# Kernel tuning notes

Hardware: AMD Instinct MI355X
Metric: run time of the kernel (lower is better)

Reference implementation:

```python
import jax, jax.numpy as jnp
import numpy as np

D, H, DK, L, FF = 512, 8, 64, 6, 2048
MAXREL = 512
R = 2 * MAXREL + 1
B, S = 4, 512


def _ln(x, g, b):
    m = jnp.mean(x, -1, keepdims=True)
    v = jnp.mean((x - m) ** 2, -1, keepdims=True)
    return (x - m) * jax.lax.rsqrt(v + 1e-5) * g + b


def _gelu(x):
    return jax.nn.gelu(x, approximate=False)


def setup_inputs() -> dict:
    key = jax.random.key(0)
    ks = iter(jax.random.split(key, 64))
    def rnd(shape, scale=0.02):
        return jax.random.normal(next(ks), shape, jnp.float32) * scale
    inp = {"x": jax.random.normal(next(ks), (B, S, D), jnp.float32)}
    # SeasonalDecomposition params (3 seasonal nets stacked on leading axis)
    inp.update(
        sd_t1_w=rnd((D, D)), sd_t1_b=jnp.zeros((D,), jnp.float32),
        sd_t2_w=rnd((D, D)), sd_t2_b=jnp.zeros((D,), jnp.float32),
        sd_s1_w=rnd((3, D, D // 2)), sd_s1_b=jnp.zeros((3, D // 2), jnp.float32),
        sd_s2_w=rnd((3, D // 2, D)), sd_s2_b=jnp.zeros((3, D), jnp.float32),
        sd_r1_w=rnd((D, D // 2)), sd_r1_b=jnp.zeros((D // 2,), jnp.float32),
        sd_r2_w=rnd((D // 2, D)), sd_r2_b=jnp.zeros((D,), jnp.float32),
        sd_comb=jnp.ones((5,), jnp.float32),
        # 6 TemporalFusionTransformer layers, params stacked on leading axis L
        wq=rnd((L, D, D)), wk=rnd((L, D, D)), wv=rnd((L, D, D)),
        wo_w=rnd((L, D, D)), wo_b=jnp.zeros((L, D), jnp.float32),
        rel_k=rnd((L, R, DK), 1.0), rel_v=rnd((L, R, DK), 1.0),
        ln_attn_g=jnp.ones((L, D), jnp.float32), ln_attn_b=jnp.zeros((L, D), jnp.float32),
        ff1_w=rnd((L, D, FF)), ff1_b=jnp.zeros((L, FF), jnp.float32),
        ff2_w=rnd((L, FF, D)), ff2_b=jnp.zeros((L, D), jnp.float32),
        n1_g=jnp.ones((L, D), jnp.float32), n1_b=jnp.zeros((L, D), jnp.float32),
        n2_g=jnp.ones((L, D), jnp.float32), n2_b=jnp.zeros((L, D), jnp.float32),
    )
    return inp


def _forward(x, sd_t1_w, sd_t1_b, sd_t2_w, sd_t2_b, sd_s1_w, sd_s1_b, sd_s2_w, sd_s2_b,
             sd_r1_w, sd_r1_b, sd_r2_w, sd_r2_b, sd_comb,
             wq, wk, wv, wo_w, wo_b, rel_k, rel_v, ln_attn_g, ln_attn_b,
             ff1_w, ff1_b, ff2_w, ff2_b, n1_g, n1_b, n2_g, n2_b):
    b, s, d = x.shape
    # relative position index matrix, rp[i, j] = clip(j - i) + MAXREL
    r = jnp.arange(s)
    rp = jnp.clip(r[None, :] - r[:, None], -MAXREL, MAXREL) + MAXREL  # [S, S]

    # ---- SeasonalDecomposition (eval mode: dropout = identity) ----
    trend = _gelu(x @ sd_t1_w + sd_t1_b) @ sd_t2_w + sd_t2_b
    h = _gelu(jnp.einsum('bsd,kdm->kbsm', x, sd_s1_w) + sd_s1_b[:, None, None, :])
    seas = jnp.einsum('kbsm,kmd->kbsd', h, sd_s2_w) + sd_s2_b[:, None, None, :]  # [3,B,S,D]
    resid = _gelu(x @ sd_r1_w + sd_r1_b) @ sd_r2_w + sd_r2_b
    w = jax.nn.softmax(sd_comb)
    x = w[0] * trend + w[4] * resid + jnp.einsum('k,kbsd->bsd', w[1:4], seas)

    scale = np.float32(1.0 / np.sqrt(DK))

    def layer(xc, p):
        q = (xc @ p['wq']).reshape(b, s, H, DK).transpose(0, 2, 1, 3)  # [B,H,S,DK]
        k = (xc @ p['wk']).reshape(b, s, H, DK).transpose(0, 2, 1, 3)
        v = (xc @ p['wv']).reshape(b, s, H, DK).transpose(0, 2, 1, 3)
        scores = jnp.einsum('bhid,bhjd->bhij', q, k) * scale
        rk = p['rel_k'][rp]  # [S,S,DK] gathered rel-pos key bias
        scores = scores + jnp.einsum('bhid,ijd->bhij', q, rk)
        a = jax.nn.softmax(scores, axis=-1)
        ctx = jnp.einsum('bhij,bhjd->bhid', a, v)
        rv = p['rel_v'][rp]  # [S,S,DK]
        ctx = ctx + jnp.einsum('bhij,ijd->bhid', a, rv)
        ctx = ctx.transpose(0, 2, 1, 3).reshape(b, s, d)
        out = ctx @ p['wo_w'] + p['wo_b']
        attn = _ln(out + xc, p['ln_attn_g'], p['ln_attn_b'])
        y = _ln(xc + attn, p['n1_g'], p['n1_b'])
        ff = _gelu(y @ p['ff1_w'] + p['ff1_b']) @ p['ff2_w'] + p['ff2_b']
        y = _ln(y + ff, p['n2_g'], p['n2_b'])
        return y, None

    layers = dict(wq=wq, wk=wk, wv=wv, wo_w=wo_w, wo_b=wo_b, rel_k=rel_k, rel_v=rel_v,
                  ln_attn_g=ln_attn_g, ln_attn_b=ln_attn_b,
                  ff1_w=ff1_w, ff1_b=ff1_b, ff2_w=ff2_w, ff2_b=ff2_b,
                  n1_g=n1_g, n1_b=n1_b, n2_g=n2_g, n2_b=n2_b)
    x, _ = jax.lax.scan(layer, x, layers)
    return x


def reference(x, sd_t1_w, sd_t1_b, sd_t2_w, sd_t2_b, sd_s1_w, sd_s1_b, sd_s2_w, sd_s2_b,
              sd_r1_w, sd_r1_b, sd_r2_w, sd_r2_b, sd_comb,
              wq, wk, wv, wo_w, wo_b, rel_k, rel_v, ln_attn_g, ln_attn_b,
              ff1_w, ff1_b, ff2_w, ff2_b, n1_g, n1_b, n2_g, n2_b):
    return _forward(x, sd_t1_w, sd_t1_b, sd_t2_w, sd_t2_b, sd_s1_w, sd_s1_b, sd_s2_w, sd_s2_b,
                    sd_r1_w, sd_r1_b, sd_r2_w, sd_r2_b, sd_comb,
                    wq, wk, wv, wo_w, wo_b, rel_k, rel_v, ln_attn_g, ln_attn_b,
                    ff1_w, ff1_b, ff2_w, ff2_b, n1_g, n1_b, n2_g, n2_b)
```

## Files before the change

kernel.cpp:

```cpp
#include <hip/hip_runtime.h>
#include <hip/hip_bf16.h>

typedef __attribute__((ext_vector_type(4))) float f32x4;
typedef __attribute__((ext_vector_type(8))) short bf16x8;
typedef __attribute__((ext_vector_type(4))) short bf16x4;

#define NL 6

static __device__ __forceinline__ unsigned short f2bf(float f) {
    __hip_bfloat16 h = __float2bfloat16(f);
    return *reinterpret_cast<unsigned short*>(&h);
}
static __device__ __forceinline__ float bf2f(unsigned short u) {
    union { unsigned int u32; float f; } c; c.u32 = ((unsigned int)u) << 16; return c.f;
}
static __device__ __forceinline__ float gelu_exact(float v) {
    return 0.5f * v * (1.0f + erff(v * 0.70710678118654752f));
}
static __device__ __forceinline__ void gload_lds16(const void* g, void* l) {
    __builtin_amdgcn_global_load_lds((const __attribute__((address_space(1))) void*)g,
                                     (__attribute__((address_space(3))) void*)l, 16, 0, 0);
}
static __device__ __forceinline__ f32x4 MF(bf16x8 a, bf16x8 b, f32x4 c) {
    return __builtin_amdgcn_mfma_f32_16x16x32_bf16(a, b, c, 0, 0, 0);
}

template<int BM, int BN, bool OBF, bool BIAS, bool GACT, bool SPART, bool DUAL, bool VTR>
__global__ __launch_bounds__(256)
void gemm3(const unsigned short* __restrict__ A, const unsigned short* __restrict__ B,
           void* __restrict__ C, unsigned short* __restrict__ C2,
           const float* __restrict__ bias,
           int M, int N, int nkt, int skN, int lda, int ldb, int ldc, float alpha,
           int modA, long sA1, long sA2, int modB, long sB1, long sB2,
           int modC, long sC1, long sC2, int biasStride, long pStride)
{
    constexpr int MI = BM / 32, NI = BN / 32;
    constexpr int ACH = BM / 8, NCH = (BM + BN) / 8;
    __shared__ __attribute__((aligned(16))) unsigned short Ls[(BM + BN) * 64];

    const int bz = blockIdx.z;
    const int sk = SPART ? (bz % skN) : 0;
    const int z  = SPART ? (bz / skN) : bz;
    const unsigned short* Ab = A + (long)(z % modA) * sA1 + (long)(z / modA) * sA2;
    const unsigned short* Bb = B + (long)(z % modB) * sB1 + (long)(z / modB) * sB2;
    const long offC = (long)(z % modC) * sC1 + (long)(z / modC) * sC2;

    const int bm0 = blockIdx.x * BM, bn0 = blockIdx.y * BN;
    const int t = threadIdx.x, lane = t & 63, w = t >> 6;
    const int wm = (w >> 1) * (BM / 2), wn = (w & 1) * (BN / 2);
    const int crow8 = lane >> 3, cs8 = lane & 7;
    const int fr = lane & 15, kq = lane >> 4;
    const int kBase = sk * nkt * 64;

    f32x4 acc[MI][NI];
    #pragma unroll
    for (int a = 0; a < MI; a++)
        #pragma unroll
        for (int b = 0; b < NI; b++) acc[a][b] = (f32x4){0.f, 0.f, 0.f, 0.f};

    for (int kt = 0; kt < nkt; ++kt) {
        const int k0 = kBase + (kt << 6);
        #pragma unroll
        for (int c0 = 0; c0 < NCH; c0 += 4) {
            int c = c0 + w;
            if (c < NCH) {
                const unsigned short* gp;
                if (c < ACH) {
                    int rit = c * 8 + crow8;
                    int ks = cs8 ^ (rit & 7);
                    gp = Ab + (long)(bm0 + rit) * lda + k0 + ks * 8;
                } else {
                    int rit = (c - ACH) * 8 + crow8;
                    int ks = cs8 ^ (rit & 7);
                    gp = Bb + (long)(bn0 + rit) * ldb + k0 + ks * 8;
                }
                gload_lds16(gp, &Ls[c * 512]);
            }
        }
        __syncthreads();
        bf16x8 af[2][MI], bfr[2][NI];
        #pragma unroll
        for (int mi = 0; mi < MI; mi++) {
            int R = wm + mi * 16 + fr;
            af[0][mi] = *(const bf16x8*)&Ls[R * 64 + ((kq ^ (R & 7)) << 3)];
            af[1][mi] = *(const bf16x8*)&Ls[R * 64 + (((4 + kq) ^ (R & 7)) << 3)];
        }
        #pragma unroll
        for (int ni = 0; ni < NI; ni++) {
            int Rb = wn + ni * 16 + fr;
            bfr[0][ni] = *(const bf16x8*)&Ls[BM * 64 + Rb * 64 + ((kq ^ (Rb & 7)) << 3)];
            bfr[1][ni] = *(const bf16x8*)&Ls[BM * 64 + Rb * 64 + (((4 + kq) ^ (Rb & 7)) << 3)];
        }
        #pragma unroll
        for (int kh = 0; kh < 2; kh++)
            #pragma unroll
            for (int mi = 0; mi < MI; mi++)
                #pragma unroll
                for (int ni = 0; ni < NI; ni++)
                    acc[mi][ni] = MF(af[kh][mi], bfr[kh][ni], acc[mi][ni]);
        __syncthreads();
    }

    const int q4 = (lane >> 4) << 2;
    if (VTR && bn0 >= 1024) {
        #pragma unroll
        for (int mi = 0; mi < MI; mi++)
            #pragma unroll
            for (int ni = 0; ni < NI; ni++)
                #pragma unroll
                for (int j = 0; j < 4; j++) {
                    int lr = wm + mi * 16 + q4 + j;
                    int lc = wn + ni * 16 + fr;
                    Ls[lc * 64 + ((((lr >> 4) ^ (lc & 3)) << 4) | (lr & 15))] = f2bf(acc[mi][ni][j]);
                }
        __syncthreads();
        int dl = t >> 2, c4 = (t & 3) << 4;
        const unsigned short* src = &Ls[dl * 64 + (((t & 3) ^ (dl & 3)) << 4)];
        unsigned short* dst = C2 + ((long)((bm0 >> 9) * 8 + ((bn0 - 1024) >> 6)) * 64 + dl) * 512
                              + (bm0 & 511) + c4;
        *(bf16x8*)dst = *(const bf16x8*)src;
        *((bf16x8*)dst + 1) = *((const bf16x8*)src + 1);
    } else if (SPART) {
        float* P = (float*)C + sk * pStride + offC;
        #pragma unroll
        for (int mi = 0; mi < MI; mi++)
            #pragma unroll
            for (int ni = 0; ni < NI; ni++)
                #pragma unroll
                for (int j = 0; j < 4; j++) {
                    int gr = bm0 + wm + mi * 16 + q4 + j;
                    int gc = bn0 + wn + ni * 16 + fr;
                    if (gc < N) P[(long)gr * ldc + gc] = acc[mi][ni][j] * alpha;
                }
    } else {
        float* Cf = (float*)C + offC;
        unsigned short* Ch = (unsigned short*)C + offC;
        unsigned short* C2h = DUAL ? (C2 + offC) : nullptr;
        const float* bp = BIAS ? (bias + (long)z * biasStride) : nullptr;
        #pragma unroll
        for (int mi = 0; mi < MI; mi++)
            #pragma unroll
            for (int ni = 0; ni < NI; ni++)
                #pragma unroll
                for (int j = 0; j < 4; j++) {
                    int gr = bm0 + wm + mi * 16 + q4 + j;
                    int gc = bn0 + wn + ni * 16 + fr;
                    if (gc < N) {
                        float v = acc[mi][ni][j] * alpha;
                        if (BIAS) v += bp[gc];
                        if (GACT) v = gelu_exact(v);
                        if (OBF) Ch[(long)gr * ldc + gc] = f2bf(v);
                        else     Cf[(long)gr * ldc + gc] = v;
                        if (DUAL) C2h[(long)gr * ldc + gc] = f2bf(v);
                    }
                }
    }
}

__global__ __launch_bounds__(256)
void fused_attn3(const unsigned short* __restrict__ qkv,
                 const unsigned short* __restrict__ vt,
                 const unsigned short* __restrict__ rk,
                 const unsigned short* __restrict__ rvt,
                 unsigned short* __restrict__ ctx)
{
    __shared__ __attribute__((aligned(16))) unsigned short L[32768];
    const int bh = blockIdx.y, b = bh >> 3, h = bh & 7;
    const int i0 = blockIdx.x * 64;
    const int t = threadIdx.x, lane = t & 63, wv = t >> 6;
    const int crow = lane >> 2, cs = lane & 3;
    const int fr = lane & 15, kq = lane >> 4;
    const int q4 = kq << 2;
    const int iiw = wv * 16;
    const int PB = 20480, GA = 24576;

    const unsigned short* Qg = qkv + ((long)(b * 512 + i0)) * 1536 + h * 64;
    const unsigned short* Kg = qkv + ((long)(b * 512)) * 1536 + 512 + h * 64;
    const unsigned short* Vg = vt + ((long)bh * 64) * 512;

    auto stage = [&](int jt, int sbuf) {
        const int j0 = jt * 64;
        const int SB = 4096 + sbuf * 8192;
        #pragma unroll
        for (int k = 0; k < 4; k++) {
            int c = wv + k * 4;
            const unsigned short* gp; int dst;
            if (c < 8) {
                int kt = c >> 2, row = (c & 3) * 16 + crow, ks = cs ^ (row & 3);
                gp = Kg + (long)(j0 + row) * 1536 + kt * 32 + ks * 8;
                dst = SB + c * 512;
            } else {
                int cc = c - 8;
                int kt = cc >> 2, row = (cc & 3) * 16 + crow, ks = cs ^ (row & 3);
                gp = Vg + (long)row * 512 + j0 + kt * 32 + ks * 8;
                dst = SB + 4096 + cc * 512;
            }
            gload_lds16(gp, &L[dst]);
        }
    };

    #pragma unroll
    for (int k = 0; k < 2; k++) {
        int c = wv + k * 4;
        int kt = c >> 2, row = (c & 3) * 16 + crow, ks = cs ^ (row & 3);
        gload_lds16(Qg + (long)row * 1536 + kt * 32 + ks * 8, &L[c * 512]);
    }
    stage(0, 0);
    __syncthreads();
    bf16x8 qf[2];
    {
        int r = iiw + fr;
        qf[0] = *(const bf16x8*)&L[r * 32 + ((kq ^ (r & 3)) << 3)];
        qf[1] = *(const bf16x8*)&L[2048 + r * 32 + ((kq ^ (r & 3)) << 3)];
    }

    f32x4 ctxa[4];
    #pragma unroll
    for (int ni = 0; ni < 4; ni++) ctxa[ni] = (f32x4){0.f, 0.f, 0.f, 0.f};
    float m_[4] = {-1e30f, -1e30f, -1e30f, -1e30f};
    float l_[4] = {0.f, 0.f, 0.f, 0.f};

    for (int jt = 0; jt < 8; ++jt) {
        const int sb = jt & 1;
        const int SB = 4096 + sb * 8192;
        const int rbase = jt * 64 - i0 + 448;
        if (jt < 7) stage(jt + 1, sb ^ 1);
        f32x4 gacc[8];
        #pragma unroll
        for (int wb = 0; wb < 8; wb++) {
            int Rb = wb * 16 + fr;
            const unsigned short* rkp = rk + (long)(rbase + Rb) * 64 + kq * 8;
            bf16x8 rk0 = *(const bf16x8*)rkp;
            bf16x8 rk1 = *(const bf16x8*)(rkp + 32);
            f32x4 g = (f32x4){0.f, 0.f, 0.f, 0.f};
            g = MF(qf[0], rk0, g);
            gacc[wb] = MF(qf[1], rk1, g);
        }
        #pragma unroll
        for (int wb = 0; wb < 8; wb++)
            #pragma unroll
            for (int j = 0; j < 4; j++) {
                int il = iiw + q4 + j, ww = wb * 16 + fr;
                L[GA + il * 128 + (((ww >> 3) ^ (il & 7)) << 3) + (ww & 7)] = f2bf(gacc[wb][j]);
            }
        f32x4 s[4];
        #pragma unroll
        for (int ni = 0; ni < 4; ni++) {
            int rB = ni * 16 + fr;
            bf16x8 b0 = *(const bf16x8*)&L[SB + rB * 32 + ((kq ^ (rB & 3)) << 3)];
            bf16x8 b1 = *(const bf16x8*)&L[SB + 2048 + rB * 32 + ((kq ^ (rB & 3)) << 3)];
            f32x4 a0 = (f32x4){0.f, 0.f, 0.f, 0.f};
            a0 = MF(qf[0], b0, a0);
            s[ni] = MF(qf[1], b1, a0);
        }
        #pragma unroll
        for (int ni = 0; ni < 4; ni++)
            #pragma unroll
            for (int j = 0; j < 4; j++) {
                int il = iiw + q4 + j;
                int ww = ni * 16 + fr - il + 64;
                s[ni][j] = s[ni][j] * 0.125f
                         + bf2f(L[GA + il * 128 + (((ww >> 3) ^ (il & 7)) << 3) + (ww & 7)]);
            }
        float mx[4];
        #pragma unroll
        for (int j = 0; j < 4; j++) {
            mx[j] = fmaxf(fmaxf(s[0][j], s[1][j]), fmaxf(s[2][j], s[3][j]));
            #pragma unroll
            for (int msk = 1; msk < 16; msk <<= 1) mx[j] = fmaxf(mx[j], __shfl_xor(mx[j], msk));
        }
        float scl[4];
        #pragma unroll
        for (int j = 0; j < 4; j++) {
            float mn = fmaxf(m_[j], mx[j]);
            scl[j] = __expf(m_[j] - mn);
            m_[j] = mn;
        }
        float rs[4] = {0.f, 0.f, 0.f, 0.f};
        #pragma unroll
        for (int ni = 0; ni < 4; ni++)
            #pragma unroll
            for (int j = 0; j < 4; j++) {
                float p = __expf(s[ni][j] - m_[j]);
                s[ni][j] = p;
                rs[j] += p;
            }
        #pragma unroll
        for (int j = 0; j < 4; j++) {
            #pragma unroll
            for (int msk = 1; msk < 16; msk <<= 1) rs[j] += __shfl_xor(rs[j], msk);
            l_[j] = l_[j] * scl[j] + rs[j];
        }
        #pragma unroll
        for (int ni = 0; ni < 4; ni++)
            #pragma unroll
            for (int j = 0; j < 4; j++) ctxa[ni][j] *= scl[j];
        #pragma unroll
        for (int ni = 0; ni < 4; ni++)
            #pragma unroll
            for (int j = 0; j < 4; j++) {
                int il = iiw + q4 + j;
                int jj = ni * 16 + fr;
                unsigned short pb = f2bf(s[ni][j]);
                L[PB + il * 64 + (((jj >> 3) ^ (il & 7)) << 3) + (jj & 7)] = pb;
                int wI = jj - il + 64;
                L[GA + il * 128 + (((wI >> 3) ^ (il & 7)) << 3) + (wI & 7)] = pb;
                int wz = (wI + 64) & 127;
                L[GA + il * 128 + (((wz >> 3) ^ (il & 7)) << 3) + (wz & 7)] = 0;
            }
        bf16x8 rvf[4][4];
        #pragma unroll
        for (int kt2 = 0; kt2 < 4; kt2++)
            #pragma unroll
            for (int ni = 0; ni < 4; ni++)
                rvf[kt2][ni] = *(const bf16x8*)(rvt + (long)(ni * 16 + fr) * 1056
                                                + rbase + kt2 * 32 + kq * 8);
        const int r = iiw + fr;
        bf16x8 pa0 = *(const bf16x8*)&L[PB + r * 64 + ((kq ^ (r & 7)) << 3)];
        bf16x8 pa1 = *(const bf16x8*)&L[PB + r * 64 + (((4 + kq) ^ (r & 7)) << 3)];
        #pragma unroll
        for (int ni = 0; ni < 4; ni++) {
            int rB = ni * 16 + fr;
            bf16x8 vb0 = *(const bf16x8*)&L[SB + 4096 + rB * 32 + ((kq ^ (rB & 3)) << 3)];
            bf16x8 vb1 = *(const bf16x8*)&L[SB + 6144 + rB * 32 + ((kq ^ (rB & 3)) << 3)];
            ctxa[ni] = MF(pa0, vb0, ctxa[ni]);
            ctxa[ni] = MF(pa1, vb1, ctxa[ni]);
        }
        #pragma unroll
        for (int kt2 = 0; kt2 < 4; kt2++) {
            bf16x8 aa = *(const bf16x8*)&L[GA + r * 128 + (((kt2 * 4 + kq) ^ (r & 7)) << 3)];
            #pragma unroll
            for (int ni = 0; ni < 4; ni++)
                ctxa[ni] = MF(aa, rvf[kt2][ni], ctxa[ni]);
        }
        __syncthreads();
    }
    #pragma unroll
    for (int j = 0; j < 4; j++) {
        float inv = 1.f / l_[j];
        int il = iiw + q4 + j;
        unsigned short* op = ctx + ((long)(b * 512 + i0 + il)) * 512 + h * 64;
        #pragma unroll
        for (int ni = 0; ni < 4; ni++)
            op[ni * 16 + fr] = f2bf(ctxa[ni][j] * inv);
    }
}

__global__ __launch_bounds__(256)
void trcast_k(const float* __restrict__ in, unsigned short* __restrict__ out,
              int R, int C, int ldo, long inStride, long outStride,
              const float* __restrict__ scp, int sczs)
{
    __shared__ unsigned short tile[32][33];
    const int z = blockIdx.z;
    const float* ip = in + (long)z * inStride;
    unsigned short* op = out + (long)z * outStride;
    const float sc = scp ? scp[z * sczs] : 1.0f;
    const int c0 = blockIdx.x * 32, r0 = blockIdx.y * 32;
    const int tx = threadIdx.x & 31, ty = threadIdx.x >> 5;
    #pragma unroll
    for (int q = 0; q < 4; q++) {
        int r = r0 + ty + q * 8;
        float v = (r < R) ? ip[(long)r * C + c0 + tx] * sc : 0.f;
        tile[ty + q * 8][tx] = f2bf(v);
    }
    __syncthreads();
    #pragma unroll
    for (int q = 0; q < 4; q++) {
        int c = c0 + ty + q * 8;
        op[(long)c * ldo + r0 + tx] = tile[tx][ty + q * 8];
    }
}

__global__ __launch_bounds__(256)
void qkvwo_tr(const float* __restrict__ wq, const float* __restrict__ wk,
              const float* __restrict__ wv, const float* __restrict__ wo,
              unsigned short* __restrict__ qkvT, unsigned short* __restrict__ woT)
{
    __shared__ unsigned short tile[32][33];
    const int z = blockIdx.z;
    const int wsel = z / 6, l = z % 6;
    const float* ip = (wsel == 0 ? wq : wsel == 1 ? wk : wsel == 2 ? wv : wo) + (long)l * 262144;
    unsigned short* op = (wsel < 3) ? (qkvT + (long)l * 786432 + (long)wsel * 262144)
                                    : (woT + (long)l * 262144);
    const int c0 = blockIdx.x * 32, r0 = blockIdx.y * 32;
    const int tx = threadIdx.x & 31, ty = threadIdx.x >> 5;
    #pragma unroll
    for (int q = 0; q < 4; q++)
        tile[ty + q * 8][tx] = f2bf(ip[(long)(r0 + ty + q * 8) * 512 + c0 + tx]);
    __syncthreads();
    #pragma unroll
    for (int q = 0; q < 4; q++)
        op[(long)(c0 + ty + q * 8) * 512 + r0 + tx] = tile[tx][ty + q * 8];
}

__global__ __launch_bounds__(256)
void castpad_k(const float* __restrict__ in, unsigned short* __restrict__ out,
               int R, int C, long inStride, long outStride, long nPerZ)
{
    const int z = blockIdx.z;
    for (long idx = (long)blockIdx.x * 256 + threadIdx.x; idx < nPerZ;
         idx += (long)gridDim.x * 256) {
        int r = (int)(idx / C);
        float v = (r < R) ? in[(long)z * inStride + idx] : 0.f;
        out[(long)z * outStride + idx] = f2bf(v);
    }
}

__global__ __launch_bounds__(256)
void ln2x_k(const float* __restrict__ p0, const float* __restrict__ p1,
            const float* __restrict__ wb, const float* __restrict__ x,
            const float* __restrict__ g1, const float* __restrict__ b1,
            const float* __restrict__ g2, const float* __restrict__ b2,
            float* __restrict__ yf, unsigned short* __restrict__ yb)
{
    const int wv = threadIdx.x >> 6, lane = threadIdx.x & 63;
    const long row = (long)blockIdx.x * 4 + wv;
    const int base = lane * 8;
    const float* pa = p0 + row * 512 + base;
    const float* pbp = p1 + row * 512 + base;
    const float* px = x + row * 512 + base;
    float xv[8], v[8];
    {
        float4 x0 = *(const float4*)px, x1 = *(const float4*)(px + 4);
        float4 a0 = *(const float4*)pa, a1 = *(const float4*)(pa + 4);
        float4 c0 = *(const float4*)pbp, c1 = *(const float4*)(pbp + 4);
        float4 w0 = *(const float4*)(wb + base), w1 = *(const float4*)(wb + base + 4);
        xv[0] = x0.x; xv[1] = x0.y; xv[2] = x0.z; xv[3] = x0.w;
        xv[4] = x1.x; xv[5] = x1.y; xv[6] = x1.z; xv[7] = x1.w;
        v[0] = xv[0] + a0.x + c0.x + w0.x; v[1] = xv[1] + a0.y + c0.y + w0.y;
        v[2] = xv[2] + a0.z + c0.z + w0.z; v[3] = xv[3] + a0.w + c0.w + w0.w;
        v[4] = xv[4] + a1.x + c1.x + w1.x; v[5] = xv[5] + a1.y + c1.y + w1.y;
        v[6] = xv[6] + a1.z + c1.z + w1.z; v[7] = xv[7] + a1.w + c1.w + w1.w;
    }
    float s = 0.f;
    #pragma unroll
    for (int jj = 0; jj < 8; jj++) s += v[jj];
    #pragma unroll
    for (int off = 32; off; off >>= 1) s += __shfl_xor(s, off);
    float mean = s * (1.f / 512.f);
    float vs = 0.f;
    #pragma unroll
    for (int jj = 0; jj < 8; jj++) { float d = v[jj] - mean; vs += d * d; }
    #pragma unroll
    for (int off = 32; off; off >>= 1) vs += __shfl_xor(vs, off);
    float inv = rsqrtf(vs * (1.f / 512.f) + 1e-5f);
    float4 ga = *(const float4*)(g1 + base), gb = *(const float4*)(g1 + base + 4);
    float4 ba = *(const float4*)(b1 + base), bb = *(const float4*)(b1 + base + 4);
    float gg[8] = {ga.x, ga.y, ga.z, ga.w, gb.x, gb.y, gb.z, gb.w};
    float ee[8] = {ba.x, ba.y, ba.z, ba.w, bb.x, bb.y, bb.z, bb.w};
    float tvec[8];
    #pragma unroll
    for (int jj = 0; jj < 8; jj++) tvec[jj] = xv[jj] + (v[jj] - mean) * inv * gg[jj] + ee[jj];
    float s2 = 0.f;
    #pragma unroll
    for (int jj = 0; jj < 8; jj++) s2 += tvec[jj];
    #pragma unroll
    for (int off = 32; off; off >>= 1) s2 += __shfl_xor(s2, off);
    float m2 = s2 * (1.f / 512.f);
    float vs2 = 0.f;
    #pragma unroll
    for (int jj = 0; jj < 8; jj++) { float d = tvec[jj] - m2; vs2 += d * d; }
    #pragma unroll
    for (int off = 32; off; off >>= 1) vs2 += __shfl_xor(vs2, off);
    float inv2 = rsqrtf(vs2 * (1.f / 512.f) + 1e-5f);
    float4 gc = *(const float4*)(g2 + base), gd = *(const float4*)(g2 + base + 4);
    float4 bc = *(const float4*)(b2 + base), bd = *(const float4*)(b2 + base + 4);
    float g2v[8] = {gc.x, gc.y, gc.z, gc.w, gd.x, gd.y, gd.z, gd.w};
    float b2v[8] = {bc.x, bc.y, bc.z, bc.w, bd.x, bd.y, bd.z, bd.w};
    float r[8];
    #pragma unroll
    for (int jj = 0; jj < 8; jj++) r[jj] = (tvec[jj] - m2) * inv2 * g2v[jj] + b2v[jj];
    float* pf = yf + row * 512 + base;
    *(float4*)pf = (float4){r[0], r[1], r[2], r[3]};
    *(float4*)(pf + 4) = (float4){r[4], r[5], r[6], r[7]};
    bf16x8 ov;
    #pragma unroll
    for (int jj = 0; jj < 8; jj++) ov[jj] = (short)f2bf(r[jj]);
    *(bf16x8*)(yb + row * 512 + base) = ov;
}

__global__ __launch_bounds__(256)
void lnff_k(const float* __restrict__ y1, const float* __restrict__ parts,
            const float* __restrict__ bias,
            const float* __restrict__ g, const float* __restrict__ be,
            float* __restrict__ o, unsigned short* __restrict__ ob)
{
    const int wv = threadIdx.x >> 6, lane = threadIdx.x & 63;
    const long row = (long)blockIdx.x * 4 + wv;
    const int base = lane * 8;
    const float* pa = y1 + row * 512 + base;
    float v[8];
    {
        float4 x0 = *(const float4*)pa, x1 = *(const float4*)(pa + 4);
        float4 w0 = *(const float4*)(bias + base), w1 = *(const float4*)(bias + base + 4);
        v[0] = x0.x + w0.x; v[1] = x0.y + w0.y; v[2] = x0.z + w0.z; v[3] = x0.w + w0.w;
        v[4] = x1.x + w1.x; v[5] = x1.y + w1.y; v[6] = x1.z + w1.z; v[7] = x1.w + w1.w;
    }
    #pragma unroll
    for (int k = 0; k < 4; k++) {
        const float* pp = parts + (long)k * 1048576 + row * 512 + base;
        float4 a0 = *(const float4*)pp, a1 = *(const float4*)(pp + 4);
        v[0] += a0.x; v[1] += a0.y; v[2] += a0.z; v[3] += a0.w;
        v[4] += a1.x; v[5] += a1.y; v[6] += a1.z; v[7] += a1.w;
    }
    float s = 0.f;
    #pragma unroll
    for (int jj = 0; jj < 8; jj++) s += v[jj];
    #pragma unroll
    for (int off = 32; off; off >>= 1) s += __shfl_xor(s, off);
    float mean = s * (1.f / 512.f);
    float vs = 0.f;
    #pragma unroll
    for (int jj = 0; jj < 8; jj++) { float d = v[jj] - mean; vs += d * d; }
    #pragma unroll
    for (int off = 32; off; off >>= 1) vs += __shfl_xor(vs, off);
    float inv = rsqrtf(vs * (1.f / 512.f) + 1e-5f);
    float4 g0 = *(const float4*)(g + base), g1 = *(const float4*)(g + base + 4);
    float4 e0 = *(const float4*)(be + base), e1 = *(const float4*)(be + base + 4);
    float gg[8] = {g0.x, g0.y, g0.z, g0.w, g1.x, g1.y, g1.z, g1.w};
    float ee[8] = {e0.x, e0.y, e0.z, e0.w, e1.x, e1.y, e1.z, e1.w};
    float r[8];
    #pragma unroll
    for (int jj = 0; jj < 8; jj++) r[jj] = (v[jj] - mean) * inv * gg[jj] + ee[jj];
    float* po = o + row * 512 + base;
    *(float4*)po = (float4){r[0], r[1], r[2], r[3]};
    *(float4*)(po + 4) = (float4){r[4], r[5], r[6], r[7]};
    bf16x8 ov;
    #pragma unroll
    for (int jj = 0; jj < 8; jj++) ov[jj] = (short)f2bf(r[jj]);
    *(bf16x8*)(ob + row * 512 + base) = ov;
}

__global__ void softmax5_k(const float* __restrict__ comb, float* __restrict__ c5)
{
    if (threadIdx.x == 0 && blockIdx.x == 0) {
        float c[5]; float m = -1e30f;
        for (int k = 0; k < 5; k++) { c[k] = comb[k]; m = fmaxf(m, c[k]); }
        float s = 0.f;
        for (int k = 0; k < 5; k++) { c[k] = __expf(c[k] - m); s += c[k]; }
        for (int k = 0; k < 5; k++) c5[k] = c[k] / s;
    }
}

__global__ __launch_bounds__(256)
void bias_build_k(const float* __restrict__ t1b, const float* __restrict__ r1b,
                  const float* __restrict__ s1b, const float* __restrict__ t2b,
                  const float* __restrict__ r2b, const float* __restrict__ s2b,
                  const float* __restrict__ c5, float* __restrict__ b1c,
                  float* __restrict__ bc)
{
    int i = threadIdx.x + blockIdx.x * 256;
    if (i < 512) b1c[i] = t1b[i];
    else if (i < 768) b1c[i] = r1b[i - 512];
    else if (i < 1536) b1c[i] = s1b[i - 768];
    else if (i < 2048) {
        int n = i - 1536;
        bc[n] = c5[0] * t2b[n] + c5[4] * r2b[n]
              + c5[1] * s2b[n] + c5[2] * s2b[512 + n] + c5[3] * s2b[1024 + n];
    }
}

#define G3(BM,BN,OBF,BIAS,GACT,SPART,DUAL,VTR, A,B,C,C2,bias_, M,N,NKT,SKN, lda,ldb,ldc, alpha, mA,a1,a2, mB,b1,b2, mC,c1,c2, bstr, pstr, Zg) \
    gemm3<BM,BN,OBF,BIAS,GACT,SPART,DUAL,VTR><<<dim3((M)/(BM), ((N)+(BN)-1)/(BN), (Zg)), dim3(256), 0, stream>>>( \
        (A),(B),(C),(C2),(bias_),(M),(N),(NKT),(SKN),(lda),(ldb),(ldc),(alpha), \
        (mA),(long)(a1),(long)(a2),(mB),(long)(b1),(long)(b2),(mC),(long)(c1),(long)(c2),(bstr),(long)(pstr))

extern "C" void kernel_launch(void* const* d_in, const int* in_sizes, int n_in,
                              void* d_out, int out_size, void* d_ws, size_t ws_size,
                              hipStream_t stream)
{
    (void)in_sizes; (void)n_in; (void)out_size; (void)ws_size;
    const float* x    = (const float*)d_in[0];
    const float* t1w  = (const float*)d_in[1];
    const float* t1b  = (const float*)d_in[2];
    const float* t2w  = (const float*)d_in[3];
    const float* t2b  = (const float*)d_in[4];
    const float* s1w  = (const float*)d_in[5];
    const float* s1b  = (const float*)d_in[6];
    const float* s2w  = (const float*)d_in[7];
    const float* s2b  = (const float*)d_in[8];
    const float* r1w  = (const float*)d_in[9];
    const float* r1b  = (const float*)d_in[10];
    const float* r2w  = (const float*)d_in[11];
    const float* r2b  = (const float*)d_in[12];
    const float* comb = (const float*)d_in[13];
    const float* wq   = (const float*)d_in[14];
    const float* wk   = (const float*)d_in[15];
    const float* wvv  = (const float*)d_in[16];
    const float* wow  = (const float*)d_in[17];
    const float* wob  = (const float*)d_in[18];
    const float* relk = (const float*)d_in[19];
    const float* relv = (const float*)d_in[20];
    const float* lag  = (const float*)d_in[21];
    const float* labi = (const float*)d_in[22];
    const float* f1w  = (const float*)d_in[23];
    const float* f1b  = (const float*)d_in[24];
    const float* f2w  = (const float*)d_in[25];
    const float* f2b  = (const float*)d_in[26];
    const float* n1g  = (const float*)d_in[27];
    const float* n1b  = (const float*)d_in[28];
    const float* n2g  = (const float*)d_in[29];
    const float* n2b  = (const float*)d_in[30];

    char* ws = (char*)d_ws;
    #define OFFK(kb) (ws + (size_t)(kb) * 1024)
    float* X    = (float*)OFFK(0);
    float* T3   = (float*)OFFK(8192);
    float* PART = (float*)OFFK(12288);
    unsigned short* Xb   = (unsigned short*)OFFK(45056);
    unsigned short* Xb0  = (unsigned short*)OFFK(47104);
    unsigned short* QKVb = (unsigned short*)OFFK(49152);
    unsigned short* VT   = (unsigned short*)OFFK(55296);
    unsigned short* CTXb = (unsigned short*)OFFK(57344);
    unsigned short* T3b  = (unsigned short*)OFFK(59392);
    unsigned short* FFb  = (unsigned short*)OFFK(61440);
    unsigned short* W1   = (unsigned short*)OFFK(69632);
    unsigned short* W2   = (unsigned short*)OFFK(71168);
    float* b1c = (float*)OFFK(72704);
    float* bc  = (float*)OFFK(72712);
    float* c5  = (float*)OFFK(72716);
    unsigned short* qkvT = (unsigned short*)OFFK(119808);
    unsigned short* woT  = (unsigned short*)OFFK(129024);
    unsigned short* f1wT = (unsigned short*)OFFK(132096);
    unsigned short* f2wT = (unsigned short*)OFFK(144384);
    unsigned short* relkb= (unsigned short*)OFFK(156672);
    unsigned short* rvT  = (unsigned short*)OFFK(157488);
    unsigned short* Hb   = QKVb;

    castpad_k<<<dim3(1024, 1, 1), 256, 0, stream>>>(x, Xb0, 2048, 512, 1048576, 1048576, 1048576);
    softmax5_k<<<dim3(1), 64, 0, stream>>>(comb, c5);
    bias_build_k<<<dim3(8), 256, 0, stream>>>(t1b, r1b, s1b, t2b, r2b, s2b, c5, b1c, bc);
    trcast_k<<<dim3(16, 16, 1), 256, 0, stream>>>(t1w, W1, 512, 512, 512, 0, 0, nullptr, 0);
    trcast_k<<<dim3(8, 16, 1), 256, 0, stream>>>(r1w, W1 + 262144, 512, 256, 512, 0, 0, nullptr, 0);
    trcast_k<<<dim3(8, 16, 3), 256, 0, stream>>>(s1w, W1 + 393216, 512, 256, 512, 131072, 131072, nullptr, 0);
    trcast_k<<<dim3(16, 16, 1), 256, 0, stream>>>(t2w, W2, 512, 512, 1536, 0, 0, c5, 0);
    trcast_k<<<dim3(16, 8, 1), 256, 0, stream>>>(r2w, W2 + 512, 256, 512, 1536, 0, 0, c5 + 4, 0);
    trcast_k<<<dim3(16, 8, 3), 256, 0, stream>>>(s2w, W2 + 768, 256, 512, 1536, 131072, 256, c5 + 1, 1);
    qkvwo_tr<<<dim3(16, 16, 24), 256, 0, stream>>>(wq, wk, wvv, wow, qkvT, woT);
    trcast_k<<<dim3(64, 16, 6), 256, 0, stream>>>(f1w, f1wT, 512, 2048, 512, 1048576, 1048576, nullptr, 0);
    trcast_k<<<dim3(16, 64, 6), 256, 0, stream>>>(f2w, f2wT, 2048, 512, 2048, 1048576, 1048576, nullptr, 0);
    trcast_k<<<dim3(2, 33, 6), 256, 0, stream>>>(relv, rvT, 1025, 64, 1056, 65600, 67584, nullptr, 0);
    castpad_k<<<dim3(272, 1, 6), 256, 0, stream>>>(relk, relkb, 1025, 64, 65600, 69632, 69632);

    G3(64,64,true,true,true,false,false,false,  Xb0, W1, Hb, nullptr, b1c, 2048,1536,8,1, 512,512,1536, 1.f,
       1,0,0, 1,0,0, 1,0,0, 0,0, 1);
    G3(64,64,false,true,false,false,true,false, Hb, W2, X, Xb, bc, 2048,512,24,1, 1536,1536,512, 1.f,
       1,0,0, 1,0,0, 1,0,0, 0,0, 1);

    for (int l = 0; l < NL; ++l) {
        const unsigned short* qkvTl = qkvT + (long)l * 786432;
        const unsigned short* woTl  = woT + (long)l * 262144;
        const unsigned short* f1Tl  = f1wT + (long)l * 1048576;
        const unsigned short* f2Tl  = f2wT + (long)l * 1048576;
        const unsigned short* rkl   = relkb + (long)l * 69632;
        const unsigned short* rvl   = rvT + (long)l * 67584;

        G3(64,64,true,false,false,false,false,true, Xb, qkvTl, QKVb, VT, nullptr, 2048,1536,8,1, 512,512,1536, 1.f,
           1,0,0, 1,0,0, 1,0,0, 0,0, 1);
        fused_attn3<<<dim3(8, 32), 256, 0, stream>>>(QKVb, VT, rkl, rvl, CTXb);
        G3(64,64,false,false,false,true,false,false, CTXb, woTl, PART, nullptr, nullptr, 2048,512,4,2, 512,512,512, 1.f,
           1,0,0, 1,0,0, 1,0,0, 0,1048576, 2);
        ln2x_k<<<dim3(512), 256, 0, stream>>>(PART, PART + 1048576, wob + l * 512, X,
                                              lag + l * 512, labi + l * 512,
                                              n1g + l * 512, n1b + l * 512, T3, T3b);
        G3(64,64,true,true,true,false,false,false, T3b, f1Tl, FFb, nullptr, f1b + l * 2048, 2048,2048,8,1, 512,512,2048, 1.f,
           1,0,0, 1,0,0, 1,0,0, 0,0, 1);
        G3(64,64,false,false,false,true,false,false, FFb, f2Tl, PART, nullptr, nullptr, 2048,512,8,4, 2048,2048,512, 1.f,
           1,0,0, 1,0,0, 1,0,0, 0,1048576, 4);
        float* outp = (l == NL - 1) ? (float*)d_out : X;
        lnff_k<<<dim3(512), 256, 0, stream>>>(T3, PART, f2b + l * 512,
                                              n2g + l * 512, n2b + l * 512, outp, Xb);
    }
}
```

Before: 596.1 us.

## Split attention over key halves with merge kernel and stage relative tables in LDS

The attention kernel is split along the key dimension into two halves via a third grid dimension, doubling block count from 256 to 512. Each half writes unnormalized fp32 partial outputs plus running max and sum, and a new merge kernel combines them into the bf16 context. Relative-key and relative-value tables are now staged into LDS with async loads instead of being read directly from global memory. Double buffering is dropped in favour of single-buffer staging with two barriers per tile. The cost is an extra launch, fp32 partial traffic and loss of load/compute overlap.

```diff
diff --git a/kernel.cpp b/kernel.cpp
--- a/kernel.cpp
+++ b/kernel.cpp
@@ -158,42 +158,52 @@
 }
 
 __global__ __launch_bounds__(256)
-void fused_attn3(const unsigned short* __restrict__ qkv,
+void fused_attn4(const unsigned short* __restrict__ qkv,
                  const unsigned short* __restrict__ vt,
                  const unsigned short* __restrict__ rk,
                  const unsigned short* __restrict__ rvt,
-                 unsigned short* __restrict__ ctx)
-{
-    __shared__ __attribute__((aligned(16))) unsigned short L[32768];
+                 float* __restrict__ op, float* __restrict__ ml)
+{
+    __shared__ __attribute__((aligned(16))) unsigned short L[40960];
     const int bh = blockIdx.y, b = bh >> 3, h = bh & 7;
     const int i0 = blockIdx.x * 64;
+    const int half = blockIdx.z;
     const int t = threadIdx.x, lane = t & 63, wv = t >> 6;
     const int crow = lane >> 2, cs = lane & 3;
     const int fr = lane & 15, kq = lane >> 4;
     const int q4 = kq << 2;
     const int iiw = wv * 16;
-    const int PB = 20480, GA = 24576;
+    const int PB = 28672, GA = 32768;
 
     const unsigned short* Qg = qkv + ((long)(b * 512 + i0)) * 1536 + h * 64;
     const unsigned short* Kg = qkv + ((long)(b * 512)) * 1536 + 512 + h * 64;
     const unsigned short* Vg = vt + ((long)bh * 64) * 512;
 
-    auto stage = [&](int jt, int sbuf) {
-        const int j0 = jt * 64;
-        const int SB = 4096 + sbuf * 8192;
-        #pragma unroll
-        for (int k = 0; k < 4; k++) {
+    auto stage = [&](int jt) {
+        const int j0 = jt * 64, rbase = j0 - i0 + 448;
+        #pragma unroll
+        for (int k = 0; k < 12; k++) {
             int c = wv + k * 4;
             const unsigned short* gp; int dst;
             if (c < 8) {
                 int kt = c >> 2, row = (c & 3) * 16 + crow, ks = cs ^ (row & 3);
                 gp = Kg + (long)(j0 + row) * 1536 + kt * 32 + ks * 8;
-                dst = SB + c * 512;
-            } else {
+                dst = 4096 + c * 512;
+            } else if (c < 16) {
                 int cc = c - 8;
                 int kt = cc >> 2, row = (cc & 3) * 16 + crow, ks = cs ^ (row & 3);
                 gp = Vg + (long)row * 512 + j0 + kt * 32 + ks * 8;
-                dst = SB + 4096 + cc * 512;
+                dst = 8192 + cc * 512;
+            } else if (c < 32) {
+                int cc = c - 16;
+                int kt = cc >> 2, row = (cc & 3) * 16 + crow, ks = cs ^ (row & 3);
+                gp = rvt + (long)row * 1056 + rbase + kt * 32 + ks * 8;
+                dst = 12288 + cc * 512;
+            } else {
+                int cc = c - 32;
+                int kt = cc >> 3, row = (cc & 7) * 16 + crow, ks = cs ^ (row & 3);
+                gp = rk + (long)(rbase + row) * 64 + kt * 32 + ks * 8;
+                dst = 20480 + cc * 512;
             }
             gload_lds16(gp, &L[dst]);
         }
@@ -205,7 +215,7 @@
         int kt = c >> 2, row = (c & 3) * 16 + crow, ks = cs ^ (row & 3);
         gload_lds16(Qg + (long)row * 1536 + kt * 32 + ks * 8, &L[c * 512]);
     }
-    stage(0, 0);
+    stage(half * 4);
     __syncthreads();
     bf16x8 qf[2];
     {
@@ -220,18 +230,16 @@
     float m_[4] = {-1e30f, -1e30f, -1e30f, -1e30f};
     float l_[4] = {0.f, 0.f, 0.f, 0.f};
 
-    for (int jt = 0; jt < 8; ++jt) {
-        const int sb = jt & 1;
-        const int SB = 4096 + sb * 8192;
+    for (int q = 0; q < 4; ++q) {
+        const int jt = half * 4 + q;
         const int rbase = jt * 64 - i0 + 448;
-        if (jt < 7) stage(jt + 1, sb ^ 1);
+        (void)rbase;
         f32x4 gacc[8];
         #pragma unroll
         for (int wb = 0; wb < 8; wb++) {
             int Rb = wb * 16 + fr;
-            const unsigned short* rkp = rk + (long)(rbase + Rb) * 64 + kq * 8;
-            bf16x8 rk0 = *(const bf16x8*)rkp;
-            bf16x8 rk1 = *(const bf16x8*)(rkp + 32);
+            bf16x8 rk0 = *(const bf16x8*)&L[20480 + Rb * 32 + ((kq ^ (Rb & 3)) << 3)];
+            bf16x8 rk1 = *(const bf16x8*)&L[24576 + Rb * 32 + ((kq ^ (Rb & 3)) << 3)];
             f32x4 g = (f32x4){0.f, 0.f, 0.f, 0.f};
             g = MF(qf[0], rk0, g);
             gacc[wb] = MF(qf[1], rk1, g);
@@ -247,8 +255,8 @@
         #pragma unroll
         for (int ni = 0; ni < 4; ni++) {
             int rB = ni * 16 + fr;
-            bf16x8 b0 = *(const bf16x8*)&L[SB + rB * 32 + ((kq ^ (rB & 3)) << 3)];
-            bf16x8 b1 = *(const bf16x8*)&L[SB + 2048 + rB * 32 + ((kq ^ (rB & 3)) << 3)];
+            bf16x8 b0 = *(const bf16x8*)&L[4096 + rB * 32 + ((kq ^ (rB & 3)) << 3)];
+            bf16x8 b1 = *(const bf16x8*)&L[6144 + rB * 32 + ((kq ^ (rB & 3)) << 3)];
             f32x4 a0 = (f32x4){0.f, 0.f, 0.f, 0.f};
             a0 = MF(qf[0], b0, a0);
             s[ni] = MF(qf[1], b1, a0);
@@ -308,21 +316,14 @@
                 int wz = (wI + 64) & 127;
                 L[GA + il * 128 + (((wz >> 3) ^ (il & 7)) << 3) + (wz & 7)] = 0;
             }
-        bf16x8 rvf[4][4];
-        #pragma unroll
-        for (int kt2 = 0; kt2 < 4; kt2++)
-            #pragma unroll
-            for (int ni = 0; ni < 4; ni++)
-                rvf[kt2][ni] = *(const bf16x8*)(rvt + (long)(ni * 16 + fr) * 1056
-                                                + rbase + kt2 * 32 + kq * 8);
         const int r = iiw + fr;
         bf16x8 pa0 = *(const bf16x8*)&L[PB + r * 64 + ((kq ^ (r & 7)) << 3)];
         bf16x8 pa1 = *(const bf16x8*)&L[PB + r * 64 + (((4 + kq) ^ (r & 7)) << 3)];
         #pragma unroll
         for (int ni = 0; ni < 4; ni++) {
             int rB = ni * 16 + fr;
-            bf16x8 vb0 = *(const bf16x8*)&L[SB + 4096 + rB * 32 + ((kq ^ (rB & 3)) << 3)];
-            bf16x8 vb1 = *(const bf16x8*)&L[SB + 6144 + rB * 32 + ((kq ^ (rB & 3)) << 3)];
+            bf16x8 vb0 = *(const bf16x8*)&L[8192 + rB * 32 + ((kq ^ (rB & 3)) << 3)];
+            bf16x8 vb1 = *(const bf16x8*)&L[10240 + rB * 32 + ((kq ^ (rB & 3)) << 3)];
             ctxa[ni] = MF(pa0, vb0, ctxa[ni]);
             ctxa[ni] = MF(pa1, vb1, ctxa[ni]);
         }
@@ -330,20 +331,50 @@
         for (int kt2 = 0; kt2 < 4; kt2++) {
             bf16x8 aa = *(const bf16x8*)&L[GA + r * 128 + (((kt2 * 4 + kq) ^ (r & 7)) << 3)];
             #pragma unroll
-            for (int ni = 0; ni < 4; ni++)
-                ctxa[ni] = MF(aa, rvf[kt2][ni], ctxa[ni]);
-        }
-        __syncthreads();
-    }
+            for (int ni = 0; ni < 4; ni++) {
+                int rB = ni * 16 + fr;
+                bf16x8 rb = *(const bf16x8*)&L[12288 + kt2 * 2048 + rB * 32 + ((kq ^ (rB & 3)) << 3)];
+                ctxa[ni] = MF(aa, rb, ctxa[ni]);
+            }
+        }
+        if (q < 3) {
+            __syncthreads();
+            stage(jt + 1);
+            __syncthreads();
+        }
+    }
+    const long prow_base = (long)half * 16384 + (long)bh * 512 + i0;
     #pragma unroll
     for (int j = 0; j < 4; j++) {
-        float inv = 1.f / l_[j];
         int il = iiw + q4 + j;
-        unsigned short* op = ctx + ((long)(b * 512 + i0 + il)) * 512 + h * 64;
+        long prow = prow_base + il;
+        float* opr = op + prow * 64;
         #pragma unroll
         for (int ni = 0; ni < 4; ni++)
-            op[ni * 16 + fr] = f2bf(ctxa[ni][j] * inv);
-    }
+            opr[ni * 16 + fr] = ctxa[ni][j];
+        if (fr == 0) {
+            ml[prow * 2] = m_[j];
+            ml[prow * 2 + 1] = l_[j];
+        }
+    }
+}
+
+__global__ __launch_bounds__(256)
+void attn_merge(const float* __restrict__ op, const float* __restrict__ ml,
+                unsigned short* __restrict__ ctx)
+{
+    const int wv = threadIdx.x >> 6, lane = threadIdx.x & 63;
+    const long row = (long)blockIdx.x * 4 + wv;
+    const int bh = (int)(row >> 9), i = (int)(row & 511);
+    const int b = bh >> 3, h = bh & 7;
+    float m0 = ml[row * 2], l0 = ml[row * 2 + 1];
+    float m1 = ml[(row + 16384) * 2], l1 = ml[(row + 16384) * 2 + 1];
+    float m = fmaxf(m0, m1);
+    float a0 = __expf(m0 - m), a1 = __expf(m1 - m);
+    float inv = 1.f / (l0 * a0 + l1 * a1);
+    float o0 = op[row * 64 + lane];
+    float o1 = op[(row + 16384) * 64 + lane];
+    ctx[((long)(b * 512 + i)) * 512 + h * 64 + lane] = f2bf((o0 * a0 + o1 * a1) * inv);
 }
 
 __global__ __launch_bounds__(256)
@@ -608,6 +639,8 @@
     float* X    = (float*)OFFK(0);
     float* T3   = (float*)OFFK(8192);
     float* PART = (float*)OFFK(12288);
+    float* OP   = PART;
+    float* ML   = PART + 2097152;
     unsigned short* Xb   = (unsigned short*)OFFK(45056);
     unsigned short* Xb0  = (unsigned short*)OFFK(47104);
     unsigned short* QKVb = (unsigned short*)OFFK(49152);
@@ -658,7 +691,8 @@
 
         G3(64,64,true,false,false,false,false,true, Xb, qkvTl, QKVb, VT, nullptr, 2048,1536,8,1, 512,512,1536, 1.f,
            1,0,0, 1,0,0, 1,0,0, 0,0, 1);
-        fused_attn3<<<dim3(8, 32), 256, 0, stream>>>(QKVb, VT, rkl, rvl, CTXb);
+        fused_attn4<<<dim3(8, 32, 2), 256, 0, stream>>>(QKVb, VT, rkl, rvl, OP, ML);
+        attn_merge<<<dim3(4096), 256, 0, stream>>>(OP, ML, CTXb);
         G3(64,64,false,false,false,true,false,false, CTXb, woTl, PART, nullptr, nullptr, 2048,512,4,2, 512,512,512, 1.f,
            1,0,0, 1,0,0, 1,0,0, 0,1048576, 2);
         ln2x_k<<<dim3(512), 256, 0, stream>>>(PART, PART + 1048576, wob + l * 512, X,
```

Result: faster. 556.6 us (-6.6%).
